# Kernel optimization log

Measured on AMD Instinct MI355X. Metric: run time of the kernel, lower is better.

The kernel has to match this reference:

```python
import jax, jax.numpy as jnp
import numpy as np

N = 16384      # total nodes in batched graph
E = 131072     # message-passing edges
E_RO = 32768   # readout edges
D = 1024       # fc7 appearance feature dim
DL = 300       # word2vec dim
DS = 16        # spatial edge feature dim
C = 117        # HICO verb classes


def setup_inputs() -> dict:
    key = jax.random.key(0)
    ks = jax.random.split(key, 20)
    s = 0.02
    return {
        'feat': jax.random.normal(ks[0], (N, D), jnp.float32),
        'word2vec': jax.random.normal(ks[1], (N, DL), jnp.float32),
        's_f': jax.random.normal(ks[2], (E, DS), jnp.float32),
        's_f_ro': jax.random.normal(ks[3], (E_RO, DS), jnp.float32),
        'W_e': jax.random.normal(ks[4], (2 * D + DS, D), jnp.float32) * s,
        'b_e': jnp.zeros((D,), jnp.float32),
        'W_el': jax.random.normal(ks[5], (2 * DL, DL), jnp.float32) * s,
        'b_el': jnp.zeros((DL,), jnp.float32),
        'W_nu': jax.random.normal(ks[6], (2 * D, D), jnp.float32) * s,
        'b_nu': jnp.zeros((D,), jnp.float32),
        'W_nul': jax.random.normal(ks[7], (2 * DL, DL), jnp.float32) * s,
        'b_nul': jnp.zeros((DL,), jnp.float32),
        'W_p': jax.random.normal(ks[8], (D + DL + DS + DL + D, C), jnp.float32) * s,
        'b_p': jnp.zeros((C,), jnp.float32),
        'edge_src': jax.random.randint(ks[9], (E,), 0, N, jnp.int32),
        'edge_dst': jax.random.randint(ks[10], (E,), 0, N, jnp.int32),
        'ro_src': jax.random.randint(ks[11], (E_RO,), 0, N, jnp.int32),
        'ro_dst': jax.random.randint(ks[12], (E_RO,), 0, N, jnp.int32),
    }


def _mean_agg(msgs, dst, n, dtype):
    # scatter-add messages to destination nodes, then mean-normalize
    summed = jax.ops.segment_sum(msgs, dst, num_segments=n)
    cnt = jax.ops.segment_sum(jnp.ones((msgs.shape[0], 1), dtype), dst, num_segments=n)
    return summed / jnp.maximum(cnt, 1.0)


def reference(feat, word2vec, s_f, s_f_ro, W_e, b_e, W_el, b_el,
              W_nu, b_nu, W_nul, b_nul, W_p, b_p,
              edge_src, edge_dst, ro_src, ro_dst):
    # --- GRNN message passing: gather -> concat -> MLP -> scatter(mean) ---
    # appearance stream: [src_feat, dst_feat, s_f] -> relu(MLP)
    m = jax.nn.relu(
        jnp.concatenate([feat[edge_src], feat[edge_dst], s_f], axis=1) @ W_e + b_e)
    agg = _mean_agg(m, edge_dst, N, feat.dtype)               # [N, D]
    # language stream: [src_w2v, dst_w2v] -> relu(MLP)
    ml = jax.nn.relu(
        jnp.concatenate([word2vec[edge_src], word2vec[edge_dst]], axis=1) @ W_el + b_el)
    aggl = _mean_agg(ml, edge_dst, N, feat.dtype)             # [N, DL]

    # --- NodeUpdate: concat(original, aggregated) -> MLP ---
    new_n_f = jax.nn.relu(jnp.concatenate([feat, agg], axis=1) @ W_nu + b_nu)
    new_n_f_lang = jax.nn.relu(
        jnp.concatenate([word2vec, aggl], axis=1) @ W_nul + b_nul)

    # --- Predictor (edge readout): concat[dst_f, dst_lang, s_f, src_lang, src_f] ---
    ef = jnp.concatenate([
        new_n_f[ro_dst], new_n_f_lang[ro_dst], s_f_ro,
        new_n_f_lang[ro_src], new_n_f[ro_src]], axis=1)       # [E_RO, 2664]
    pred = ef @ W_p + b_p                                     # [E_RO, 117]
    return pred
```

## Files before the change

### kernel.cpp

```cpp
#include <hip/hip_runtime.h>

typedef unsigned short u16;
typedef __attribute__((ext_vector_type(8))) short short8;
typedef __attribute__((ext_vector_type(4))) float f32x4;

#define NN 16384
#define EE 131072
#define ERO 32768
#define DF 1024
#define DL 300
#define DLP 320
#define DLN 384
#define DS 16
#define NC 117
#define NCP 128

__device__ __forceinline__ float bf2f(u16 x) {
  unsigned int u = ((unsigned int)x) << 16;
  float f;
  __builtin_memcpy(&f, &u, 4);
  return f;
}
__device__ __forceinline__ u16 f2bf(float f) {
  unsigned int u;
  __builtin_memcpy(&u, &f, 4);
  u = (u + 0x7FFFu + ((u >> 16) & 1u)) >> 16;
  return (u16)u;
}
__device__ __forceinline__ float ld1(const void* p, size_t i, int f) {
  return f ? ((const float*)p)[i] : bf2f(((const u16*)p)[i]);
}
__device__ __forceinline__ void ld4(const void* p, size_t i, int f,
                                    float& x, float& y, float& z, float& w) {
  if (f) {
    float4 v = *(const float4*)((const float*)p + i);
    x = v.x; y = v.y; z = v.z; w = v.w;
  } else {
    ushort4 v = *(const ushort4*)((const u16*)p + i);
    x = bf2f(v.x); y = bf2f(v.y); z = bf2f(v.z); w = bf2f(v.w);
  }
}
__device__ __forceinline__ const void* eoff(const void* p, size_t off, int f) {
  return f ? (const void*)((const float*)p + off) : (const void*)((const u16*)p + off);
}

__global__ void detect_kernel(const unsigned int* __restrict__ w, int* __restrict__ flag) {
  unsigned int x = w[threadIdx.x];
  int e = (x >> 7) & 0xFF;
  int ok = (e >= 97 && e <= 157);
  unsigned long long m = __ballot(ok);
  if (threadIdx.x == 0) flag[0] = (__popcll(m) >= 48) ? 0 : 1;
}

__global__ void cast_bf16(const int* __restrict__ flag, const void* __restrict__ src,
                          u16* __restrict__ dst, int total8) {
  const int i = blockIdx.x * 256 + threadIdx.x;
  if (i >= total8) return;
  const int fin = flag[0];
  const size_t o = (size_t)i * 8;
  float x0, x1, x2, x3, x4, x5, x6, x7;
  ld4(src, o, fin, x0, x1, x2, x3);
  ld4(src, o + 4, fin, x4, x5, x6, x7);
  ushort4 lo, hi;
  lo.x = f2bf(x0); lo.y = f2bf(x1); lo.z = f2bf(x2); lo.w = f2bf(x3);
  hi.x = f2bf(x4); hi.y = f2bf(x5); hi.z = f2bf(x6); hi.w = f2bf(x7);
  *(ushort4*)(dst + o) = lo;
  *(ushort4*)(dst + o + 4) = hi;
}

struct TJob {
  const void* W; long off;
  int Kr, Nr, Nstr, Kp, Np, blk0;
};
struct TPack { TJob j[12]; int nj; };

__global__ void prep_weights(const int* __restrict__ flag, TPack P, u16* __restrict__ outbase,
                             const long* __restrict__ outoffs_unused) {
}

struct TJob2 {
  const void* W; long off;
  u16* out;
  int Kr, Nr, Nstr, Kp, Np, blk0;
};
struct TPack2 { TJob2 j[12]; int nj; };

__global__ void prep_weights2(const int* __restrict__ flag, TPack2 P) {
  int b = blockIdx.x;
  int ji = 0;
  while (ji + 1 < P.nj && b >= P.j[ji + 1].blk0) ++ji;
  const TJob2 J = P.j[ji];
  const int idx = (b - J.blk0) * 256 + threadIdx.x;
  if (idx >= J.Np * J.Kp) return;
  const int n = idx / J.Kp, k = idx % J.Kp;
  float v = 0.f;
  if (k < J.Kr && n < J.Nr) v = ld1(J.W, (size_t)J.off + (size_t)k * J.Nstr + n, flag[0]);
  J.out[idx] = f2bf(v);
}

__device__ __forceinline__ void stage_bf16_async(const u16* __restrict__ G, size_t rbase,
                                                 int lda, int k0, u16* lds, int w, int lane) {
  #pragma unroll
  for (int t = 0; t < 2; ++t) {
    const int rr = (w << 5) + (t << 4) + (lane >> 2);
    const u16* gp = G + (rbase + rr) * (size_t)lda + k0 + ((lane & 3) << 3);
    __builtin_amdgcn_global_load_lds(
        (const __attribute__((address_space(1))) void*)gp,
        (__attribute__((address_space(3))) void*)(lds + (((w << 5) + (t << 4)) * 32)),
        16, 0, 0);
  }
}

__device__ __forceinline__ void stage_f32_manual(const float* __restrict__ G, int row0,
                                                 int lda, int k0, int Kreal,
                                                 u16* lds, int tid) {
  const int r = tid >> 1, half = tid & 1;
  const float* gp = G + (size_t)(row0 + r) * lda + k0 + (half << 4);
  #pragma unroll
  for (int qq = 0; qq < 4; ++qq) {
    const int kk = k0 + (half << 4) + (qq << 2);
    float4 v = make_float4(0.f, 0.f, 0.f, 0.f);
    if (kk < Kreal) v = *(const float4*)(gp + (qq << 2));
    ushort4 o;
    o.x = f2bf(v.x); o.y = f2bf(v.y); o.z = f2bf(v.z); o.w = f2bf(v.w);
    *(ushort4*)(lds + r * 32 + (half << 4) + (qq << 2)) = o;
  }
}

__device__ __forceinline__ void kloop(int am, const void* __restrict__ A, int lda,
                                      int Kreal, int Kpad, const u16* __restrict__ B,
                                      u16* As, u16* Bs, f32x4 (&acc)[4][4],
                                      int row0, int col0,
                                      int tid, int lane, int w, int wm, int wn, int ml, int q) {
  for (int k0 = 0; k0 < Kpad; k0 += 32) {
    if (am == 0) stage_bf16_async((const u16*)A, (size_t)row0, lda, k0, As, w, lane);
    else         stage_f32_manual((const float*)A, row0, lda, k0, Kreal, As, tid);
    stage_bf16_async(B, (size_t)col0, Kpad, k0, Bs, w, lane);
    __syncthreads();
    short8 af[4], bfr[4];
    #pragma unroll
    for (int i = 0; i < 4; ++i)
      af[i] = *(const short8*)(As + ((wm << 6) + (i << 4) + ml) * 32 + (q << 3));
    #pragma unroll
    for (int j = 0; j < 4; ++j)
      bfr[j] = *(const short8*)(Bs + ((wn << 6) + (j << 4) + ml) * 32 + (q << 3));
    #pragma unroll
    for (int i = 0; i < 4; ++i)
      #pragma unroll
      for (int j = 0; j < 4; ++j)
        acc[i][j] = __builtin_amdgcn_mfma_f32_16x16x32_bf16(af[i], bfr[j], acc[i][j], 0, 0, 0);
    __syncthreads();
  }
}

struct GJob {
  const void* A1; const u16* B1;
  const void* A2; const u16* B2;
  const void* bias; void* C;
  int lda1, K1real, K1pad, am1;
  int lda2, K2real, K2pad, am2;
  int inBias, ldc, Nreal, Npad, relu, cf32;
  int gx, gy, blk0;
};
struct GPack { GJob j[2]; int nj; };

__global__ __launch_bounds__(256) void mfma_jobs(const int* __restrict__ flag, GPack P) {
  const int b = blockIdx.x;
  int ji = 0;
  if (P.nj > 1 && b >= P.j[1].blk0) ji = 1;
  const GJob J = P.j[ji];
  const int t = b - J.blk0;
  const int xcd = t & 7, s = t >> 3;
  const int row_t = xcd * (J.gy >> 3) + s / J.gx;
  const int col_t = s % J.gx;
  const int row0 = row_t << 7;
  const int col0 = col_t << 7;

  __shared__ __attribute__((aligned(16))) u16 As[128 * 32];
  __shared__ __attribute__((aligned(16))) u16 Bs[128 * 32];
  const int tid = threadIdx.x;
  const int lane = tid & 63;
  const int w = tid >> 6;
  const int wm = w >> 1, wn = w & 1;
  const int ml = lane & 15, q = lane >> 4;

  f32x4 acc[4][4];
  #pragma unroll
  for (int i = 0; i < 4; ++i)
    #pragma unroll
    for (int j = 0; j < 4; ++j) {
      f32x4 z = {0.f, 0.f, 0.f, 0.f};
      acc[i][j] = z;
    }

  kloop(J.am1, J.A1, J.lda1, J.K1real, J.K1pad, J.B1, As, Bs, acc,
        row0, col0, tid, lane, w, wm, wn, ml, q);
  if (J.am2 >= 0)
    kloop(J.am2, J.A2, J.lda2, J.K2real, J.K2pad, J.B2, As, Bs, acc,
          row0, col0, tid, lane, w, wm, wn, ml, q);

  const int fin = flag[0];
  #pragma unroll
  for (int j = 0; j < 4; ++j) {
    const int col = col0 + (wn << 6) + (j << 4) + ml;
    if (col >= J.Npad) continue;
    float bv = 0.f;
    if (J.bias && col < J.Nreal) bv = ld1(J.bias, col, J.inBias ? fin : 0);
    #pragma unroll
    for (int i = 0; i < 4; ++i) {
      #pragma unroll
      for (int r = 0; r < 4; ++r) {
        const int row = row0 + (wm << 6) + (i << 4) + (q << 2) + r;
        float v = 0.f;
        if (col < J.Nreal) {
          v = acc[i][j][r] + bv;
          if (J.relu) v = fmaxf(v, 0.f);
        }
        if (J.cf32) ((float*)J.C)[(size_t)row * J.ldc + col] = v;
        else        ((u16*)J.C)[(size_t)row * J.ldc + col] = f2bf(v);
      }
    }
  }
}

__global__ void cnt_kernel(const int* __restrict__ edst, int* __restrict__ cnt) {
  const int i = blockIdx.x * 256 + threadIdx.x;
  if (i < EE) atomicAdd(&cnt[edst[i]], 1);
}

__global__ __launch_bounds__(1024) void scan_kernel(const int* __restrict__ cnt,
                                                    int* __restrict__ offs,
                                                    int* __restrict__ woffs) {
  __shared__ int part[1024];
  const int t = threadIdx.x;
  const int base = t * 16;
  int loc[16];
  int s = 0;
  #pragma unroll
  for (int i = 0; i < 16; ++i) { loc[i] = s; s += cnt[base + i]; }
  part[t] = s;
  __syncthreads();
  for (int off = 1; off < 1024; off <<= 1) {
    int v = (t >= off) ? part[t - off] : 0;
    __syncthreads();
    part[t] += v;
    __syncthreads();
  }
  const int chunk_excl = (t == 0) ? 0 : part[t - 1];
  #pragma unroll
  for (int i = 0; i < 16; ++i) {
    int o = chunk_excl + loc[i];
    offs[base + i] = o;
    woffs[base + i] = o;
  }
  if (t == 1023) offs[NN] = part[1023];
}

__global__ void scatter_kernel(const int* __restrict__ esrc, const int* __restrict__ edst,
                               int* __restrict__ woffs,
                               int* __restrict__ order, int* __restrict__ srcs) {
  const int e = blockIdx.x * 256 + threadIdx.x;
  if (e < EE) {
    const int d = edst[e];
    const int pos = atomicAdd(&woffs[d], 1);
    order[pos] = e;
    srcs[pos] = esrc[e];
  }
}

__global__ __launch_bounds__(256) void app_agg(
    const int* __restrict__ flag,
    const u16* __restrict__ P12, const void* __restrict__ s_f,
    const void* __restrict__ W_eb, const void* __restrict__ b_e,
    const int* __restrict__ offs, const int* __restrict__ order,
    const int* __restrict__ srcs, u16* __restrict__ aggn)
{
  const int fin = flag[0];
  const int n = blockIdx.x;
  const int tid = threadIdx.x;
  const int c4 = tid << 2;
  const void* W_es = eoff(W_eb, (size_t)2 * DF * DF, fin);

  float wx[16], wy[16], wz[16], ww[16];
  #pragma unroll
  for (int k = 0; k < 16; ++k)
    ld4(W_es, (size_t)k * DF + c4, fin, wx[k], wy[k], wz[k], ww[k]);

  float be0, be1, be2, be3;
  ld4(b_e, c4, fin, be0, be1, be2, be3);
  const ushort4 p2 = *(const ushort4*)(P12 + (size_t)n * 2048 + 1024 + c4);
  const float base0 = bf2f(p2.x) + be0;
  const float base1 = bf2f(p2.y) + be1;
  const float base2 = bf2f(p2.z) + be2;
  const float base3 = bf2f(p2.w) + be3;

  const int beg = offs[n], end = offs[n + 1];
  float a0 = 0.f, a1 = 0.f, a2 = 0.f, a3 = 0.f;
  int j = beg;
  for (; j + 4 <= end; j += 4) {
    int ee[4], ss[4];
    #pragma unroll
    for (int m = 0; m < 4; ++m) { ee[m] = order[j + m]; ss[m] = srcs[j + m]; }
    float u0[4], u1[4], u2[4], u3[4], sfv[4][16];
    #pragma unroll
    for (int m = 0; m < 4; ++m) {
      #pragma unroll
      for (int k = 0; k < 16; k += 4)
        ld4(s_f, (size_t)ee[m] * DS + k, fin,
            sfv[m][k], sfv[m][k + 1], sfv[m][k + 2], sfv[m][k + 3]);
      const ushort4 pm = *(const ushort4*)(P12 + (size_t)ss[m] * 2048 + c4);
      u0[m] = bf2f(pm.x) + base0;
      u1[m] = bf2f(pm.y) + base1;
      u2[m] = bf2f(pm.z) + base2;
      u3[m] = bf2f(pm.w) + base3;
    }
    #pragma unroll
    for (int k = 0; k < 16; ++k)
      #pragma unroll
      for (int m = 0; m < 4; ++m) {
        u0[m] = fmaf(sfv[m][k], wx[k], u0[m]);
        u1[m] = fmaf(sfv[m][k], wy[k], u1[m]);
        u2[m] = fmaf(sfv[m][k], wz[k], u2[m]);
        u3[m] = fmaf(sfv[m][k], ww[k], u3[m]);
      }
    #pragma unroll
    for (int m = 0; m < 4; ++m) {
      a0 += fmaxf(u0[m], 0.f); a1 += fmaxf(u1[m], 0.f);
      a2 += fmaxf(u2[m], 0.f); a3 += fmaxf(u3[m], 0.f);
    }
  }
  for (; j < end; ++j) {
    const int e = order[j], s = srcs[j];
    float sf[16];
    #pragma unroll
    for (int k = 0; k < 16; k += 4)
      ld4(s_f, (size_t)e * DS + k, fin, sf[k], sf[k + 1], sf[k + 2], sf[k + 3]);
    const ushort4 p1 = *(const ushort4*)(P12 + (size_t)s * 2048 + c4);
    float v0 = bf2f(p1.x) + base0;
    float v1 = bf2f(p1.y) + base1;
    float v2 = bf2f(p1.z) + base2;
    float v3 = bf2f(p1.w) + base3;
    #pragma unroll
    for (int k = 0; k < 16; ++k) {
      v0 = fmaf(sf[k], wx[k], v0);
      v1 = fmaf(sf[k], wy[k], v1);
      v2 = fmaf(sf[k], wz[k], v2);
      v3 = fmaf(sf[k], ww[k], v3);
    }
    a0 += fmaxf(v0, 0.f); a1 += fmaxf(v1, 0.f);
    a2 += fmaxf(v2, 0.f); a3 += fmaxf(v3, 0.f);
  }
  const float inv = 1.f / fmaxf((float)(end - beg), 1.f);
  ushort4 o;
  o.x = f2bf(a0 * inv); o.y = f2bf(a1 * inv);
  o.z = f2bf(a2 * inv); o.w = f2bf(a3 * inv);
  *(ushort4*)(aggn + (size_t)n * DF + c4) = o;
}

__global__ __launch_bounds__(320) void lang_agg(
    const int* __restrict__ flag,
    const u16* __restrict__ Q12, const void* __restrict__ b_el,
    const int* __restrict__ offs, const int* __restrict__ srcs,
    u16* __restrict__ aggln)
{
  const int fin = flag[0];
  const int n = blockIdx.x;
  const int c = threadIdx.x;
  if (c >= DL) { aggln[(size_t)n * DLP + c] = 0; return; }
  const float base = bf2f(Q12[(size_t)n * 768 + 384 + c]) + ld1(b_el, c, fin);
  const int beg = offs[n], end = offs[n + 1];
  float s0 = 0.f, s1 = 0.f, s2 = 0.f, s3 = 0.f;
  int j = beg;
  for (; j + 4 <= end; j += 4) {
    s0 += fmaxf(bf2f(Q12[(size_t)srcs[j] * 768 + c]) + base, 0.f);
    s1 += fmaxf(bf2f(Q12[(size_t)srcs[j + 1] * 768 + c]) + base, 0.f);
    s2 += fmaxf(bf2f(Q12[(size_t)srcs[j + 2] * 768 + c]) + base, 0.f);
    s3 += fmaxf(bf2f(Q12[(size_t)srcs[j + 3] * 768 + c]) + base, 0.f);
  }
  for (; j < end; ++j) s0 += fmaxf(bf2f(Q12[(size_t)srcs[j] * 768 + c]) + base, 0.f);
  const float a = (s0 + s1) + (s2 + s3);
  aggln[(size_t)n * DLP + c] = f2bf(a / fmaxf((float)(end - beg), 1.f));
}

__global__ __launch_bounds__(256) void readout_kernel(
    const int* __restrict__ flag,
    const float* __restrict__ RdRs,
    const void* __restrict__ s_f_ro,
    const void* __restrict__ W_pb, size_t offWps,
    const void* __restrict__ b_p,
    const int* __restrict__ rsrc, const int* __restrict__ rdst, void* __restrict__ out)
{
  const int fin = flag[0];
  __shared__ float wps[16 * NC];
  const void* Wp_s = eoff(W_pb, offWps, fin);
  const int tid = threadIdx.x;
  for (int i = tid; i < 16 * NC; i += 256) wps[i] = ld1(Wp_s, i, fin);
  __syncthreads();
  const int slot = tid >> 7;
  const int c = tid & 127;
  const float bp = (c < NC) ? ld1(b_p, c, fin) : 0.f;

  const int e0 = (blockIdx.x << 3) + slot;
  #pragma unroll
  for (int ee = 0; ee < 8; ee += 2) {
    const int e = e0 + ee;
    const int s = rsrc[e];
    const int d = rdst[e];
    if (c < NC) {
      float acc = RdRs[(size_t)d * 256 + c] + RdRs[(size_t)s * 256 + 128 + c] + bp;
      #pragma unroll
      for (int k = 0; k < 16; ++k)
        acc = fmaf(ld1(s_f_ro, (size_t)e * DS + k, fin), wps[k * NC + c], acc);
      if (fin) ((float*)out)[(size_t)e * NC + c] = acc;
      else     ((u16*)out)[(size_t)e * NC + c] = f2bf(acc);
    }
  }
}

extern "C" void kernel_launch(void* const* d_in, const int* in_sizes, int n_in,
                              void* d_out, int out_size, void* d_ws, size_t ws_size,
                              hipStream_t stream)
{
  const void* feat  = d_in[0];
  const void* w2v   = d_in[1];
  const void* s_f   = d_in[2];
  const void* s_fro = d_in[3];
  const void* W_e   = d_in[4];
  const void* b_e   = d_in[5];
  const void* W_el  = d_in[6];
  const void* b_el  = d_in[7];
  const void* W_nu  = d_in[8];
  const void* b_nu  = d_in[9];
  const void* W_nul = d_in[10];
  const void* b_nul = d_in[11];
  const void* W_p   = d_in[12];
  const void* b_p   = d_in[13];
  const int* esrc  = (const int*)d_in[14];
  const int* edst  = (const int*)d_in[15];
  const int* rsrc  = (const int*)d_in[16];
  const int* rdst  = (const int*)d_in[17];

  char* p = (char*)d_ws;
  int* flag  = (int*)p; p += 256;
  int* cnt   = (int*)p; p += (size_t)NN * 4;
  int* offs  = (int*)p; p += (size_t)(NN + 64) * 4;
  int* woffs = (int*)p; p += (size_t)NN * 4;
  int* order = (int*)p; p += (size_t)EE * 4;
  int* srcs  = (int*)p; p += (size_t)EE * 4;
  u16* featB  = (u16*)p; p += (size_t)NN * DF * 2;
  u16* We12T  = (u16*)p; p += (size_t)2 * DF * DF * 2;
  u16* Wnu1T  = (u16*)p; p += (size_t)DF * DF * 2;
  u16* Wnu2T  = (u16*)p; p += (size_t)DF * DF * 2;
  u16* Wel12T = (u16*)p; p += (size_t)2 * DLN * DLP * 2;
  u16* Wnul1T = (u16*)p; p += (size_t)DLN * DLP * 2;
  u16* Wnul2T = (u16*)p; p += (size_t)DLN * DLP * 2;
  u16* WpFT2  = (u16*)p; p += (size_t)2 * NCP * DF * 2;
  u16* WpLT2  = (u16*)p; p += (size_t)2 * NCP * DLP * 2;
  u16* P12   = (u16*)p; p += (size_t)NN * 2048 * 2;
  u16* Q12   = (u16*)p; p += (size_t)NN * 768 * 2;
  u16* aggln = (u16*)p; p += (size_t)NN * DLP * 2;
  u16* aggn  = (u16*)p; p += (size_t)NN * DF * 2;
  u16* newf = P12;
  u16* newl = P12 + (size_t)NN * DF;
  float* RdRs = (float*)Q12;

  detect_kernel<<<1, 64, 0, stream>>>((const unsigned int*)feat, flag);
  hipMemsetAsync(cnt, 0, (size_t)NN * 4, stream);
  cast_bf16<<<(NN * DF / 8 + 255) / 256, 256, 0, stream>>>(flag, feat, featB, NN * DF / 8);

  TPack2 tp{};
  int tb = 0, tn = 0;
  auto T = [&](const void* W, long off, int Kr, int Nr, int Nstr, u16* out, int Kp, int Np) {
    tp.j[tn] = TJob2{W, off, out, Kr, Nr, Nstr, Kp, Np, tb};
    tb += (Np * Kp + 255) / 256;
    ++tn;
  };
  T(W_e,   0,                   DF, DF, DF, We12T,                     DF, DF);
  T(W_e,   (long)DF * DF,       DF, DF, DF, We12T + (size_t)DF * DF,   DF, DF);
  T(W_nu,  0,                   DF, DF, DF, Wnu1T, DF, DF);
  T(W_nu,  (long)DF * DF,       DF, DF, DF, Wnu2T, DF, DF);
  T(W_el,  0,                   DL, DL, DL, Wel12T,                     DLP, DLN);
  T(W_el,  (long)DL * DL,       DL, DL, DL, Wel12T + (size_t)DLN * DLP, DLP, DLN);
  T(W_nul, 0,                   DL, DL, DL, Wnul1T, DLP, DLN);
  T(W_nul, (long)DL * DL,       DL, DL, DL, Wnul2T, DLP, DLN);
  T(W_p,   0,                                DF, NC, NC, WpFT2,                     DF,  NCP);
  T(W_p,   (long)(DF + DL + DS + DL) * NC,   DF, NC, NC, WpFT2 + (size_t)NCP * DF,  DF,  NCP);
  T(W_p,   (long)DF * NC,                    DL, NC, NC, WpLT2,                     DLP, NCP);
  T(W_p,   (long)(DF + DL + DS) * NC,        DL, NC, NC, WpLT2 + (size_t)NCP * DLP, DLP, NCP);
  tp.nj = tn;
  prep_weights2<<<tb, 256, 0, stream>>>(flag, tp);

  cnt_kernel<<<EE / 256, 256, 0, stream>>>(edst, cnt);
  scan_kernel<<<1, 1024, 0, stream>>>(cnt, offs, woffs);
  scatter_kernel<<<EE / 256, 256, 0, stream>>>(esrc, edst, woffs, order, srcs);

  {
    GPack g{};
    g.j[0] = GJob{featB, We12T, nullptr, nullptr, nullptr, P12,
                  DF, DF, DF, 0,    0, 0, 0, -1,
                  0, 2048, 2048, 2048, 0, 0,  16, 128, 0};
    g.j[1] = GJob{w2v, Wel12T, nullptr, nullptr, nullptr, Q12,
                  DL, DL, DLP, 1,   0, 0, 0, -1,
                  0, 768, 768, 768, 0, 0,    6, 128, 2048};
    g.nj = 2;
    mfma_jobs<<<2048 + 768, 256, 0, stream>>>(flag, g);
  }

  lang_agg<<<NN, DLP, 0, stream>>>(flag, Q12, b_el, offs, srcs, aggln);
  app_agg<<<NN, 256, 0, stream>>>(flag, P12, s_f, W_e, b_e, offs, order, srcs, aggn);

  {
    GPack g{};
    g.j[0] = GJob{featB, Wnu1T, aggn, Wnu2T, b_nu, newf,
                  DF, DF, DF, 0,    DF, DF, DF, 0,
                  1, DF, DF, DF, 1, 0,       8, 128, 0};
    g.j[1] = GJob{w2v, Wnul1T, aggln, Wnul2T, b_nul, newl,
                  DL, DL, DLP, 1,   DLP, DLP, DLP, 0,
                  1, DLP, DL, DLP, 1, 0,     3, 128, 1024};
    g.nj = 2;
    mfma_jobs<<<1024 + 384, 256, 0, stream>>>(flag, g);
  }

  {
    GPack g{};
    g.j[0] = GJob{newf, WpFT2, newl, WpLT2, nullptr, RdRs,
                  DF, DF, DF, 0,    DLP, DLP, DLP, 0,
                  0, 256, 256, 256, 0, 1,    2, 128, 0};
    g.nj = 1;
    mfma_jobs<<<256, 256, 0, stream>>>(flag, g);
  }

  readout_kernel<<<ERO / 8, 256, 0, stream>>>(flag, RdRs, s_fro,
                                              W_p, (size_t)(DF + DL) * NC, b_p,
                                              rsrc, rdst, d_out);
}
```

Before: 656.3 us.

## Store GEMM tiles in LDS in MFMA fragment order and pack bf16 output stores

Result: slower. 772.7 us (+17.7%).

```diff
diff --git a/kernel.cpp b/kernel.cpp
--- a/kernel.cpp
+++ b/kernel.cpp
@@ -68,16 +68,6 @@
   *(ushort4*)(dst + o + 4) = hi;
 }
 
-struct TJob {
-  const void* W; long off;
-  int Kr, Nr, Nstr, Kp, Np, blk0;
-};
-struct TPack { TJob j[12]; int nj; };
-
-__global__ void prep_weights(const int* __restrict__ flag, TPack P, u16* __restrict__ outbase,
-                             const long* __restrict__ outoffs_unused) {
-}
-
 struct TJob2 {
   const void* W; long off;
   u16* out;
@@ -98,32 +88,44 @@
   J.out[idx] = f2bf(v);
 }
 
-__device__ __forceinline__ void stage_bf16_async(const u16* __restrict__ G, size_t rbase,
+__device__ __forceinline__ void stage_frag_async(const u16* __restrict__ G, size_t rcbase,
                                                  int lda, int k0, u16* lds, int w, int lane) {
   #pragma unroll
   for (int t = 0; t < 2; ++t) {
-    const int rr = (w << 5) + (t << 4) + (lane >> 2);
-    const u16* gp = G + (rbase + rr) * (size_t)lda + k0 + ((lane & 3) << 3);
+    const int sg = (w << 1) + t;
+    const int row = ((sg >> 2) << 6) + ((sg & 3) << 4) + (lane & 15);
+    const u16* gp = G + (rcbase + row) * (size_t)lda + k0 + ((lane >> 4) << 3);
     __builtin_amdgcn_global_load_lds(
         (const __attribute__((address_space(1))) void*)gp,
-        (__attribute__((address_space(3))) void*)(lds + (((w << 5) + (t << 4)) * 32)),
+        (__attribute__((address_space(3))) void*)(lds + sg * 512),
         16, 0, 0);
   }
 }
 
-__device__ __forceinline__ void stage_f32_manual(const float* __restrict__ G, int row0,
-                                                 int lda, int k0, int Kreal,
-                                                 u16* lds, int tid) {
-  const int r = tid >> 1, half = tid & 1;
-  const float* gp = G + (size_t)(row0 + r) * lda + k0 + (half << 4);
-  #pragma unroll
-  for (int qq = 0; qq < 4; ++qq) {
-    const int kk = k0 + (half << 4) + (qq << 2);
-    float4 v = make_float4(0.f, 0.f, 0.f, 0.f);
-    if (kk < Kreal) v = *(const float4*)(gp + (qq << 2));
-    ushort4 o;
-    o.x = f2bf(v.x); o.y = f2bf(v.y); o.z = f2bf(v.z); o.w = f2bf(v.w);
-    *(ushort4*)(lds + r * 32 + (half << 4) + (qq << 2)) = o;
+__device__ __forceinline__ void stage_f32_frag(const float* __restrict__ G, int row0,
+                                               int lda, int k0, int Kreal,
+                                               u16* lds, int tid) {
+  const int row = tid >> 1;
+  const int q0 = (tid & 1) << 1;
+  const int sg = ((row >> 6) << 2) + ((row >> 4) & 3);
+  const int r15 = row & 15;
+  const float* gr = G + (size_t)(row0 + row) * lda;
+  #pragma unroll
+  for (int qq = 0; qq < 2; ++qq) {
+    const int q = q0 + qq;
+    const int kk = k0 + (q << 3);
+    float4 v0 = make_float4(0.f, 0.f, 0.f, 0.f);
+    float4 v1 = make_float4(0.f, 0.f, 0.f, 0.f);
+    if (kk < Kreal) {
+      v0 = *(const float4*)(gr + kk);
+      if (kk + 4 < Kreal) v1 = *(const float4*)(gr + kk + 4);
+    }
+    u16* dst = lds + sg * 512 + (((q << 4) + r15) << 3);
+    ushort4 a, b;
+    a.x = f2bf(v0.x); a.y = f2bf(v0.y); a.z = f2bf(v0.z); a.w = f2bf(v0.w);
+    b.x = f2bf(v1.x); b.y = f2bf(v1.y); b.z = f2bf(v1.z); b.w = f2bf(v1.w);
+    *(ushort4*)dst = a;
+    *(ushort4*)(dst + 4) = b;
   }
 }
 
@@ -131,19 +133,20 @@
                                       int Kreal, int Kpad, const u16* __restrict__ B,
                                       u16* As, u16* Bs, f32x4 (&acc)[4][4],
                                       int row0, int col0,
-                                      int tid, int lane, int w, int wm, int wn, int ml, int q) {
+                                      int tid, int lane, int w, int wm, int wn) {
+  const int lo8 = lane << 3;
   for (int k0 = 0; k0 < Kpad; k0 += 32) {
-    if (am == 0) stage_bf16_async((const u16*)A, (size_t)row0, lda, k0, As, w, lane);
-    else         stage_f32_manual((const float*)A, row0, lda, k0, Kreal, As, tid);
-    stage_bf16_async(B, (size_t)col0, Kpad, k0, Bs, w, lane);
+    if (am == 0) stage_frag_async((const u16*)A, (size_t)row0, lda, k0, As, w, lane);
+    else         stage_f32_frag((const float*)A, row0, lda, k0, Kreal, As, tid);
+    stage_frag_async(B, (size_t)col0, Kpad, k0, Bs, w, lane);
     __syncthreads();
     short8 af[4], bfr[4];
     #pragma unroll
     for (int i = 0; i < 4; ++i)
-      af[i] = *(const short8*)(As + ((wm << 6) + (i << 4) + ml) * 32 + (q << 3));
+      af[i] = *(const short8*)(As + (((wm << 2) + i) << 9) + lo8);
     #pragma unroll
     for (int j = 0; j < 4; ++j)
-      bfr[j] = *(const short8*)(Bs + ((wn << 6) + (j << 4) + ml) * 32 + (q << 3));
+      bfr[j] = *(const short8*)(Bs + (((wn << 2) + j) << 9) + lo8);
     #pragma unroll
     for (int i = 0; i < 4; ++i)
       #pragma unroll
@@ -194,10 +197,10 @@
     }
 
   kloop(J.am1, J.A1, J.lda1, J.K1real, J.K1pad, J.B1, As, Bs, acc,
-        row0, col0, tid, lane, w, wm, wn, ml, q);
+        row0, col0, tid, lane, w, wm, wn);
   if (J.am2 >= 0)
     kloop(J.am2, J.A2, J.lda2, J.K2real, J.K2pad, J.B2, As, Bs, acc,
-          row0, col0, tid, lane, w, wm, wn, ml, q);
+          row0, col0, tid, lane, w, wm, wn);
 
   const int fin = flag[0];
   #pragma unroll
@@ -216,8 +219,16 @@
           v = acc[i][j][r] + bv;
           if (J.relu) v = fmaxf(v, 0.f);
         }
-        if (J.cf32) ((float*)J.C)[(size_t)row * J.ldc + col] = v;
-        else        ((u16*)J.C)[(size_t)row * J.ldc + col] = f2bf(v);
+        if (J.cf32) {
+          ((float*)J.C)[(size_t)row * J.ldc + col] = v;
+        } else {
+          unsigned mine = f2bf(v);
+          unsigned other = (unsigned)__shfl_xor((int)mine, 1, 64);
+          if (!(lane & 1)) {
+            unsigned word = mine | (other << 16);
+            *(unsigned*)((u16*)J.C + (size_t)row * J.ldc + (col & ~1)) = word;
+          }
+        }
       }
     }
   }
```
